# Optimization experiments

Hardware: AMD Instinct MI355X
Metric: run time of the kernel (lower is better)

Reference implementation:

```python
import jax, jax.numpy as jnp
import numpy as np

BIG = 1e10  # sentinel distance used by the original code


def _index_points(points, idx):
    # points: [B,N,C], idx: [B,N,8] -> [B,N,8,C]
    return jax.vmap(lambda p, i: p[i])(points, idx)


def _pointsift_select(radius, xyz):
    """Octant-wise nearest neighbor within radius. xyz: [B,N,3] -> idx int32 [B,N,8]."""
    B, N, _ = xyz.shape
    judge = radius ** 2
    # diff[b,n,p] = xyz[b,p] - xyz[b,n]
    diff = xyz[:, None, :, :] - xyz[:, :, None, :]            # [B,N,N,3]
    dist = jnp.sum(diff * diff, axis=-1)                      # [B,N,N]
    # octant code: ((p - n) + 1) truncated to int, dotted with [4,2,1]
    octw = jnp.array([4, 2, 1], dtype=jnp.int32)
    code = jnp.sum((diff + 1.0).astype(jnp.int32) * octw, axis=-1)  # [B,N,N]
    diag = jnp.eye(N, dtype=bool)[None]                       # self entry -> judge_dist
    idx_per_oct = []
    for i in range(8):
        d = jnp.where((code == i) & (dist > 1e-10) & (dist < judge), dist, BIG)
        d = jnp.where(diag, judge, d)
        idx_per_oct.append(jnp.argmin(d, axis=-1))            # first-min, matches torch.min
    return jnp.stack(idx_per_oct, axis=-1).astype(jnp.int32)  # [B,N,8]


def setup_inputs() -> dict:
    key = jax.random.key(0)
    k1, k2 = jax.random.split(key)
    B, N, C = 2, 4096, 64
    xyz = jax.random.uniform(k1, (B, N, 3), dtype=jnp.float32)
    points = jax.random.normal(k2, (B, N, C), dtype=jnp.float32)
    return {"xyz": xyz, "points": points, "radius": 0.25}


def reference(xyz, points, radius):
    B, N, _ = xyz.shape
    idx = _pointsift_select(radius, xyz)                      # [B,N,8]
    grouped_xyz = _index_points(xyz, idx) - xyz[:, :, None, :]  # [B,N,8,3]
    grouped_feats = _index_points(points, idx)                # [B,N,8,C]
    grouped_points = jnp.concatenate([grouped_xyz, grouped_feats], axis=-1)  # use_xyz=True
    return grouped_xyz, grouped_points, idx
```

## Files before the change

### kernel.cpp

```cpp
#include <hip/hip_runtime.h>

#define BB 2
#define NN 4096
#define CC 64
#define QPB 4
#define TPQ 64
#define NT 256

#define OUT0_OFF 0
#define OUT1_OFF (BB * NN * 8 * 3)
#define OUT2_OFF (OUT1_OFF + BB * NN * 8 * 67)

#define WS_SORTED_BYTES (BB * NN * 16)

__global__ __launch_bounds__(1024) void build_grid(
    const float* __restrict__ xyz, float4* __restrict__ sorted,
    int* __restrict__ offsets)
{
    __shared__ int hist[64];
    __shared__ int offs[65];
    const int b = blockIdx.x;
    const int tid = threadIdx.x;
    if (tid < 64) hist[tid] = 0;
    __syncthreads();
    const float* src = xyz + (size_t)b * NN * 3;
    #pragma unroll
    for (int p = tid; p < NN; p += 1024) {
        float x = src[p * 3 + 0], y = src[p * 3 + 1], z = src[p * 3 + 2];
        int cell = (((int)(x * 4.0f)) << 4) | (((int)(y * 4.0f)) << 2)
                 | ((int)(z * 4.0f));
        atomicAdd(&hist[cell], 1);
    }
    __syncthreads();
    if (tid < 64) {
        int inc = hist[tid];
        #pragma unroll
        for (int d = 1; d < 64; d <<= 1) {
            int u = __shfl_up(inc, d, 64);
            if (tid >= d) inc += u;
        }
        offs[tid + 1] = inc;
        if (tid == 0) offs[0] = 0;
    }
    __syncthreads();
    if (tid < 65) offsets[b * 65 + tid] = offs[tid];
    if (tid < 64) hist[tid] = offs[tid];
    __syncthreads();
    float4* dst = sorted + (size_t)b * NN;
    #pragma unroll
    for (int p = tid; p < NN; p += 1024) {
        float x = src[p * 3 + 0], y = src[p * 3 + 1], z = src[p * 3 + 2];
        int cell = (((int)(x * 4.0f)) << 4) | (((int)(y * 4.0f)) << 2)
                 | ((int)(z * 4.0f));
        int pos = atomicAdd(&hist[cell], 1);
        dst[pos] = make_float4(x, y, z, __uint_as_float((unsigned)p));
    }
}

__global__ __launch_bounds__(NT, 8) void select_gather(
    const float4* __restrict__ sorted, const int* __restrict__ offsets,
    const float* __restrict__ xyz, const float* __restrict__ points,
    const float* __restrict__ radius_p, float* __restrict__ out)
{
    __shared__ int s_off[65];
    __shared__ unsigned long long s_sb[QPB * 8];

    const int tid = threadIdx.x;
    const int blk = blockIdx.x;
    const int b = blk >> 10;
    const int qslot = (blk & 1023) * QPB;
    const float4* sb = sorted + (size_t)b * NN;

    if (tid < 65) s_off[tid] = offsets[b * 65 + tid];

    const float r = radius_p[0];
    const float judge = __fmul_rn(r, r);
    const unsigned OFFC = __float_as_uint(1e-10f) + 1u;
    const unsigned seedkey = __float_as_uint(judge) - OFFC;

    const int g = tid >> 6;
    const float4 q = sb[qslot + g];
    const unsigned n = __float_as_uint(q.w);
    const float qx = q.x, qy = q.y, qz = q.z;
    const int sub = tid & 63;

    const unsigned long long seed64 = ((unsigned long long)seedkey << 32) | n;
    if (sub < 8) s_sb[g * 8 + sub] = seed64;

    const int lx = max(0, (int)((qx - r) * 4.0f));
    const int hx = min(3, (int)((qx + r) * 4.0f));
    const int ly = max(0, (int)((qy - r) * 4.0f));
    const int hy = min(3, (int)((qy + r) * 4.0f));
    const int lz = max(0, (int)((qz - r) * 4.0f));
    const int hz = min(3, (int)((qz + r) * 4.0f));

    __syncthreads();

    for (int cx = lx; cx <= hx; ++cx) {
        for (int cy = ly; cy <= hy; ++cy) {
            const int cb = (cx << 4) | (cy << 2);
            const int s = s_off[cb + lz];
            const int e = s_off[cb + hz + 1];
            #pragma unroll 2
            for (int p = s + sub; p < e; p += TPQ) {
                float4 c = sb[p];
                float dx = __fsub_rn(c.x, qx);
                float dy = __fsub_rn(c.y, qy);
                float dz = __fsub_rn(c.z, qz);
                float dist = __fadd_rn(__fadd_rn(__fmul_rn(dx, dx),
                                                 __fmul_rn(dy, dy)),
                                       __fmul_rn(dz, dz));
                if (dist < judge) {
                    unsigned ikey = __float_as_uint(dist) - OFFC;
                    int code = (((int)__fadd_rn(dx, 1.0f)) * 4 +
                                ((int)__fadd_rn(dy, 1.0f)) * 2 +
                                ((int)__fadd_rn(dz, 1.0f)));
                    atomicMin(&s_sb[g * 8 + code],
                              ((unsigned long long)ikey << 32) |
                              (unsigned long long)__float_as_uint(c.w));
                }
            }
        }
    }

    unsigned idx8[8];
    #pragma unroll
    for (int o = 0; o < 8; ++o)
        idx8[o] = (unsigned)(s_sb[g * 8 + o] & 0xFFFFFFFFull);

    const size_t tb = ((size_t)b * NN + n) * 8;
    if (sub < 8)
        out[OUT2_OFF + tb + sub] = (float)idx8[sub];

    const float* xb = xyz + (size_t)b * NN * 3;
    const float* pb = points + (size_t)b * NN * CC;
    const float qc = (sub == 0) ? qx : ((sub == 1) ? qy : qz);
    #pragma unroll
    for (int o = 0; o < 8; ++o) {
        const int i = (int)idx8[o];
        const size_t t = tb + o;
        float v;
        if (sub < 3) v = __fsub_rn(xb[i * 3 + sub], qc);
        else         v = pb[(size_t)i * CC + (sub - 3)];
        __builtin_nontemporal_store(v, &out[OUT1_OFF + t * 67 + sub]);
        if (sub >= 61)
            __builtin_nontemporal_store(pb[(size_t)i * CC + sub],
                                        &out[OUT1_OFF + t * 67 + (sub + 3)]);
        if (sub < 3)
            __builtin_nontemporal_store(v, &out[OUT0_OFF + t * 3 + sub]);
    }
}

extern "C" void kernel_launch(void* const* d_in, const int* in_sizes, int n_in,
                              void* d_out, int out_size, void* d_ws, size_t ws_size,
                              hipStream_t stream) {
    const float* xyz    = (const float*)d_in[0];
    const float* points = (const float*)d_in[1];
    const float* radius = (const float*)d_in[2];
    float* out = (float*)d_out;
    float4* ws_sorted = (float4*)d_ws;
    int* ws_offsets = (int*)((char*)d_ws + WS_SORTED_BYTES);

    hipLaunchKernelGGL(build_grid, dim3(BB), dim3(1024), 0, stream,
                       xyz, ws_sorted, ws_offsets);
    hipLaunchKernelGGL(select_gather,
                       dim3(BB * (NN / QPB)), dim3(NT), 0, stream,
                       ws_sorted, ws_offsets, xyz, points, radius, out);
}
```

Baseline: 91.68 us.

## Process two adjacent sorted queries per wavefront sharing candidate loads

Each wavefront now handles two spatially adjacent queries from the sorted order and scans the union of their grid cell ranges. Each candidate point is loaded once and tested against both queries, cutting global loads and loop overhead per query, and the grid has half as many blocks. In exchange, the union bounding box can cover more cells than either query needs, which adds distance work. Occupancy hints change to allow more registers per thread.

```diff
diff --git a/kernel.cpp b/kernel.cpp
--- a/kernel.cpp
+++ b/kernel.cpp
@@ -3,8 +3,7 @@
 #define BB 2
 #define NN 4096
 #define CC 64
-#define QPB 4
-#define TPQ 64
+#define QPW 2
 #define NT 256
 
 #define OUT0_OFF 0
@@ -57,18 +56,20 @@
     }
 }
 
-__global__ __launch_bounds__(NT, 8) void select_gather(
+__global__ __launch_bounds__(NT, 4) void select_gather(
     const float4* __restrict__ sorted, const int* __restrict__ offsets,
     const float* __restrict__ xyz, const float* __restrict__ points,
     const float* __restrict__ radius_p, float* __restrict__ out)
 {
     __shared__ int s_off[65];
-    __shared__ unsigned long long s_sb[QPB * 8];
+    __shared__ unsigned long long s_sb[4 * QPW * 8];
 
     const int tid = threadIdx.x;
     const int blk = blockIdx.x;
-    const int b = blk >> 10;
-    const int qslot = (blk & 1023) * QPB;
+    const int b = blk >> 9;
+    const int wid = tid >> 6;
+    const int sub = tid & 63;
+    const int qslot = ((blk & 511) * 4 + wid) * QPW;
     const float4* sb = sorted + (size_t)b * NN;
 
     if (tid < 65) s_off[tid] = offsets[b * 65 + tid];
@@ -78,21 +79,21 @@
     const unsigned OFFC = __float_as_uint(1e-10f) + 1u;
     const unsigned seedkey = __float_as_uint(judge) - OFFC;
 
-    const int g = tid >> 6;
-    const float4 q = sb[qslot + g];
-    const unsigned n = __float_as_uint(q.w);
-    const float qx = q.x, qy = q.y, qz = q.z;
-    const int sub = tid & 63;
+    const float4 q0 = sb[qslot + 0];
+    const float4 q1 = sb[qslot + 1];
+    const unsigned n0 = __float_as_uint(q0.w);
+    const unsigned n1 = __float_as_uint(q1.w);
 
-    const unsigned long long seed64 = ((unsigned long long)seedkey << 32) | n;
-    if (sub < 8) s_sb[g * 8 + sub] = seed64;
+    unsigned long long* wsb = s_sb + wid * (QPW * 8);
+    if (sub < 8)       wsb[sub]     = ((unsigned long long)seedkey << 32) | n0;
+    else if (sub < 16) wsb[sub]     = ((unsigned long long)seedkey << 32) | n1;
 
-    const int lx = max(0, (int)((qx - r) * 4.0f));
-    const int hx = min(3, (int)((qx + r) * 4.0f));
-    const int ly = max(0, (int)((qy - r) * 4.0f));
-    const int hy = min(3, (int)((qy + r) * 4.0f));
-    const int lz = max(0, (int)((qz - r) * 4.0f));
-    const int hz = min(3, (int)((qz + r) * 4.0f));
+    const int lx = max(0, (int)((fminf(q0.x, q1.x) - r) * 4.0f));
+    const int hx = min(3, (int)((fmaxf(q0.x, q1.x) + r) * 4.0f));
+    const int ly = max(0, (int)((fminf(q0.y, q1.y) - r) * 4.0f));
+    const int hy = min(3, (int)((fmaxf(q0.y, q1.y) + r) * 4.0f));
+    const int lz = max(0, (int)((fminf(q0.z, q1.z) - r) * 4.0f));
+    const int hz = min(3, (int)((fmaxf(q0.z, q1.z) + r) * 4.0f));
 
     __syncthreads();
 
@@ -101,53 +102,77 @@
             const int cb = (cx << 4) | (cy << 2);
             const int s = s_off[cb + lz];
             const int e = s_off[cb + hz + 1];
-            #pragma unroll 2
-            for (int p = s + sub; p < e; p += TPQ) {
+            #pragma unroll 4
+            for (int p = s + sub; p < e; p += 64) {
                 float4 c = sb[p];
-                float dx = __fsub_rn(c.x, qx);
-                float dy = __fsub_rn(c.y, qy);
-                float dz = __fsub_rn(c.z, qz);
-                float dist = __fadd_rn(__fadd_rn(__fmul_rn(dx, dx),
-                                                 __fmul_rn(dy, dy)),
-                                       __fmul_rn(dz, dz));
-                if (dist < judge) {
-                    unsigned ikey = __float_as_uint(dist) - OFFC;
-                    int code = (((int)__fadd_rn(dx, 1.0f)) * 4 +
-                                ((int)__fadd_rn(dy, 1.0f)) * 2 +
-                                ((int)__fadd_rn(dz, 1.0f)));
-                    atomicMin(&s_sb[g * 8 + code],
-                              ((unsigned long long)ikey << 32) |
-                              (unsigned long long)__float_as_uint(c.w));
+                const unsigned long long ci =
+                    (unsigned long long)__float_as_uint(c.w);
+                {
+                    float dx = __fsub_rn(c.x, q0.x);
+                    float dy = __fsub_rn(c.y, q0.y);
+                    float dz = __fsub_rn(c.z, q0.z);
+                    float dist = __fadd_rn(__fadd_rn(__fmul_rn(dx, dx),
+                                                     __fmul_rn(dy, dy)),
+                                           __fmul_rn(dz, dz));
+                    if (dist < judge) {
+                        unsigned ikey = __float_as_uint(dist) - OFFC;
+                        int code = (((int)__fadd_rn(dx, 1.0f)) * 4 +
+                                    ((int)__fadd_rn(dy, 1.0f)) * 2 +
+                                    ((int)__fadd_rn(dz, 1.0f)));
+                        atomicMin(&wsb[code],
+                                  ((unsigned long long)ikey << 32) | ci);
+                    }
+                }
+                {
+                    float dx = __fsub_rn(c.x, q1.x);
+                    float dy = __fsub_rn(c.y, q1.y);
+                    float dz = __fsub_rn(c.z, q1.z);
+                    float dist = __fadd_rn(__fadd_rn(__fmul_rn(dx, dx),
+                                                     __fmul_rn(dy, dy)),
+                                           __fmul_rn(dz, dz));
+                    if (dist < judge) {
+                        unsigned ikey = __float_as_uint(dist) - OFFC;
+                        int code = (((int)__fadd_rn(dx, 1.0f)) * 4 +
+                                    ((int)__fadd_rn(dy, 1.0f)) * 2 +
+                                    ((int)__fadd_rn(dz, 1.0f)));
+                        atomicMin(&wsb[8 + code],
+                                  ((unsigned long long)ikey << 32) | ci);
+                    }
                 }
             }
         }
     }
 
-    unsigned idx8[8];
-    #pragma unroll
-    for (int o = 0; o < 8; ++o)
-        idx8[o] = (unsigned)(s_sb[g * 8 + o] & 0xFFFFFFFFull);
-
-    const size_t tb = ((size_t)b * NN + n) * 8;
-    if (sub < 8)
-        out[OUT2_OFF + tb + sub] = (float)idx8[sub];
-
     const float* xb = xyz + (size_t)b * NN * 3;
     const float* pb = points + (size_t)b * NN * CC;
-    const float qc = (sub == 0) ? qx : ((sub == 1) ? qy : qz);
     #pragma unroll
-    for (int o = 0; o < 8; ++o) {
-        const int i = (int)idx8[o];
-        const size_t t = tb + o;
-        float v;
-        if (sub < 3) v = __fsub_rn(xb[i * 3 + sub], qc);
-        else         v = pb[(size_t)i * CC + (sub - 3)];
-        __builtin_nontemporal_store(v, &out[OUT1_OFF + t * 67 + sub]);
-        if (sub >= 61)
-            __builtin_nontemporal_store(pb[(size_t)i * CC + sub],
-                                        &out[OUT1_OFF + t * 67 + (sub + 3)]);
-        if (sub < 3)
-            __builtin_nontemporal_store(v, &out[OUT0_OFF + t * 3 + sub]);
+    for (int qq = 0; qq < QPW; ++qq) {
+        const unsigned n = qq ? n1 : n0;
+        const float4 q = qq ? q1 : q0;
+        unsigned idx8[8];
+        #pragma unroll
+        for (int o = 0; o < 8; ++o)
+            idx8[o] = (unsigned)(wsb[qq * 8 + o] & 0xFFFFFFFFull);
+
+        const size_t tb = ((size_t)b * NN + n) * 8;
+        if (sub < 8)
+            out[OUT2_OFF + tb + sub] = (float)idx8[sub];
+
+        const float qc = (sub == 0) ? q.x : ((sub == 1) ? q.y : q.z);
+        #pragma unroll
+        for (int o = 0; o < 8; ++o) {
+            const int i = (int)idx8[o];
+            const size_t t = tb + o;
+            float v;
+            if (sub < 3) v = __fsub_rn(xb[i * 3 + sub], qc);
+            else         v = pb[(size_t)i * CC + (sub - 3)];
+            __builtin_nontemporal_store(v, &out[OUT1_OFF + t * 67 + sub]);
+            if (sub >= 61)
+                __builtin_nontemporal_store(pb[(size_t)i * CC + sub],
+                                            &out[OUT1_OFF + t * 67 + (sub + 3)]);
+            if (sub < 3)
+                __builtin_nontemporal_store(v, &out[OUT0_OFF + t * 3 + sub]);
+        }
     }
 }
 
@@ -164,6 +189,6 @@
     hipLaunchKernelGGL(build_grid, dim3(BB), dim3(1024), 0, stream,
                        xyz, ws_sorted, ws_offsets);
     hipLaunchKernelGGL(select_gather,
-                       dim3(BB * (NN / QPB)), dim3(NT), 0, stream,
+                       dim3(BB * (NN / (4 * QPW))), dim3(NT), 0, stream,
                        ws_sorted, ws_offsets, xyz, points, radius, out);
 }
```

Result: slower. 99.87 us (+8.9%).
